# Performance work log

Hardware: AMD Instinct MI355X
Metric: run time of the kernel (lower is better)

## Reference

```python
import jax, jax.numpy as jnp
import numpy as np

T, D, N, K, H = 4096, 2560, 8, 4, 256
QUERY_PRE_ATTN_SCALAR = 256.0
ROPE_THETA = 10000.0
RMS_EPS = 1e-6
SLIDING_WINDOW = 1024
NEG_INF = -1e30


def setup_inputs() -> dict:
    key = jax.random.key(0)
    ks = jax.random.split(key, 6)
    return {
        "x": jax.random.normal(ks[0], (T, D), dtype=jnp.float32),
        "wq": jax.random.normal(ks[1], (D, N, H), dtype=jnp.float32) * 0.02,
        "wk": jax.random.normal(ks[2], (D, K, H), dtype=jnp.float32) * 0.02,
        "wv": jax.random.normal(ks[3], (D, K, H), dtype=jnp.float32) * 0.02,
        "wo": jax.random.normal(ks[4], (N, H, D), dtype=jnp.float32) * 0.02,
        "q_norm_w": jnp.ones((H,), dtype=jnp.float32),
        "k_norm_w": jnp.ones((H,), dtype=jnp.float32),
        "positions": jnp.arange(T, dtype=jnp.int32),
    }


def rms_norm(x, w, eps=RMS_EPS):
    rms = jnp.sqrt(jnp.mean(x * x, axis=-1, keepdims=True) + eps)
    return w * (x / rms)


def apply_rope(x, positions, head_dim, theta):
    # x: [T, heads, H]; rotate-half RoPE
    half = head_dim // 2
    inv_freq = theta ** (-(jnp.arange(half, dtype=jnp.float32) * 2.0 / head_dim))
    ang = positions.astype(jnp.float32)[:, None] * inv_freq  # [T, half]
    sin = jnp.sin(ang)[:, None, :]
    cos = jnp.cos(ang)[:, None, :]
    x1, x2 = jnp.split(x, 2, axis=-1)
    return jnp.concatenate([x1 * cos - x2 * sin, x2 * cos + x1 * sin], axis=-1)


def reference(x, wq, wk, wv, wo, q_norm_w, k_norm_w, positions):
    # QKV projections (per-head)
    q = jnp.einsum('td,dnh->tnh', x, wq)            # [T, N, H]
    q = rms_norm(q, q_norm_w)
    q = q * (QUERY_PRE_ATTN_SCALAR ** -0.5)
    q = apply_rope(q, positions, H, ROPE_THETA)

    k = jnp.einsum('td,dkh->tkh', x, wk)            # [T, K, H]
    k = rms_norm(k, k_norm_w)
    k = apply_rope(k, positions, H, ROPE_THETA)

    v = jnp.einsum('td,dkh->tkh', x, wv)            # [T, K, H]

    # GQA sliding-window causal attention
    G = N // K
    qh = q.reshape(T, K, G, H)
    scores = jnp.einsum('tkgh,skh->kgts', qh, k)    # [K, G, T, T]
    pq = positions[:, None]
    pk = positions[None, :]
    mask = (pk <= pq) & (pq - pk < SLIDING_WINDOW)  # [T, T]
    scores = jnp.where(mask, scores, NEG_INF)
    p = jax.nn.softmax(scores, axis=-1)
    attn = jnp.einsum('kgts,skh->tkgh', p, v).reshape(T, N, H)

    o = jnp.einsum('tnh,nhd->td', attn, wo)         # [T, D]
    new_kv_cache = jnp.stack([k, v])                # [2, T, K, H]
    return new_kv_cache, o
```

## Files before the change

### kernel.cpp

```cpp
#include <hip/hip_runtime.h>
#include <stdint.h>

#define T_TOK 4096
#define DM    2560
#define NQ    8
#define NKV   4
#define HD    256
#define WIN   1024

using bf16x8 = __attribute__((ext_vector_type(8))) short;
using f32x4  = __attribute__((ext_vector_type(4))) float;
typedef unsigned short u16;

__device__ __forceinline__ u16 f2bf(float x) {
  union { float f; uint32_t u; } v; v.f = x;
  uint32_t u = v.u;
  return (u16)((u + 0x7fffu + ((u >> 16) & 1u)) >> 16);
}
__device__ __forceinline__ float bf2f(u16 b) {
  union { uint32_t u; float f; } v; v.u = ((uint32_t)b) << 16;
  return v.f;
}

__device__ __forceinline__ void async_cp16(const void* g, void* lds) {
  __builtin_amdgcn_global_load_lds(
      (const __attribute__((address_space(1))) uint32_t*)(uintptr_t)g,
      (__attribute__((address_space(3))) uint32_t*)(uint32_t)(uintptr_t)lds,
      16, 0, 0);
}

__global__ __launch_bounds__(256) void convert_f32_bf16(
    const float* __restrict__ in, u16* __restrict__ out, int n)
{
  for (int i = (blockIdx.x * 256 + threadIdx.x) * 8; i < n; i += gridDim.x * 256 * 8) {
    float4 a = *(const float4*)(in + i);
    float4 b = *(const float4*)(in + i + 4);
    bf16x8 o;
    o[0] = (short)f2bf(a.x); o[1] = (short)f2bf(a.y);
    o[2] = (short)f2bf(a.z); o[3] = (short)f2bf(a.w);
    o[4] = (short)f2bf(b.x); o[5] = (short)f2bf(b.y);
    o[6] = (short)f2bf(b.z); o[7] = (short)f2bf(b.w);
    *(bf16x8*)(out + i) = o;
  }
}

__global__ __launch_bounds__(256) void transpose_f32_bf16(
    const float* __restrict__ in, u16* __restrict__ out, int R, int C)
{
  __shared__ u16 tile[64][72];
  const int r0 = blockIdx.y * 64, c0 = blockIdx.x * 64;
  const int tr = threadIdx.x >> 6, tc = threadIdx.x & 63;
  #pragma unroll
  for (int i = 0; i < 16; ++i) {
    int r = tr + i * 4;
    tile[r][tc] = f2bf(in[(size_t)(r0 + r) * C + c0 + tc]);
  }
  __syncthreads();
  const int oc = threadIdx.x >> 3, ch = threadIdx.x & 7;
  #pragma unroll
  for (int h = 0; h < 2; ++h) {
    const int c = oc + h * 32;
    bf16x8 v;
    #pragma unroll
    for (int j = 0; j < 8; ++j) v[j] = (short)tile[ch * 8 + j][c];
    *(bf16x8*)(out + (size_t)(c0 + c) * R + r0 + ch * 8) = v;
  }
}

template<bool F32OUT>
__global__ __launch_bounds__(512, 1) void gemm256p(
    const u16* __restrict__ A, const u16* __restrict__ B, void* __restrict__ Cv,
    int Kd, int lda, int ldb, int ldc)
{
  __shared__ __align__(16) u16 lds[2][2][256 * 64];
  const int tid = threadIdx.x;
  const int wave = tid >> 6, lane = tid & 63;
  const int lg = lane >> 4, lc = lane & 15;
  const int wr = wave >> 2, wc = wave & 3;
  const int nwg = gridDim.x, bid = blockIdx.x;
  const int nid = (bid & 7) * (nwg >> 3) + (bid >> 3);
  const int m0 = (nid & 15) * 256, n0 = (nid >> 4) * 256;
  const int NT = Kd >> 6;

  const int srow = tid >> 3;
  const int scol = ((tid & 7) * 16) ^ ((srow & 7) << 4);
  const u16* Ag = A + (size_t)(m0 + srow) * lda + (scol >> 1);
  const u16* Bg = B + (size_t)(n0 + srow) * ldb + (scol >> 1);

  #define STAGE_B4(BUF, KT) do {                                              \
    const int kc_ = (KT) * 64;                                                \
    _Pragma("unroll")                                                         \
    for (int li = 0; li < 4; ++li)                                            \
      async_cp16(Bg + (size_t)(li * 64) * ldb + kc_,                          \
                 (char*)&lds[BUF][1][0] + li * 8192 + wave * 1024);           \
  } while (0)
  #define STAGE_A2(BUF, KT, H) do {                                           \
    const int kc_ = (KT) * 64;                                                \
    async_cp16(Ag + (size_t)((H) * 64) * lda + kc_,                           \
               (char*)&lds[BUF][0][0] + (H) * 8192 + wave * 1024);            \
    async_cp16(Ag + (size_t)((H) * 64 + 128) * lda + kc_,                     \
               (char*)&lds[BUF][0][0] + ((H) + 2) * 8192 + wave * 1024);      \
  } while (0)
  #define LOAD_AF(P) do {                                                     \
    _Pragma("unroll")                                                         \
    for (int im = 0; im < 2; ++im)                                            \
      _Pragma("unroll")                                                       \
      for (int k2 = 0; k2 < 2; ++k2) {                                        \
        const int row = wr * 128 + ((P) * 2 + im) * 16 + lc;                  \
        const int cb = k2 * 64 + lg * 16;                                     \
        af[im][k2] = *(const bf16x8*)(Ab + row * 128 + (cb ^ ((row & 7) << 4))); \
      }                                                                       \
  } while (0)
  #define MFMA_Q(P) do {                                                      \
    __builtin_amdgcn_s_setprio(1);                                            \
    _Pragma("unroll")                                                         \
    for (int im = 0; im < 2; ++im)                                            \
      _Pragma("unroll")                                                       \
      for (int j = 0; j < 4; ++j)                                             \
        _Pragma("unroll")                                                     \
        for (int k2 = 0; k2 < 2; ++k2)                                        \
          acc[(P) * 2 + im][j] = __builtin_amdgcn_mfma_f32_16x16x32_bf16(     \
              af[im][k2], bfr[j][k2], acc[(P) * 2 + im][j], 0, 0, 0);         \
    __builtin_amdgcn_s_setprio(0);                                            \
  } while (0)
  #define LGKM0_BAR() do {                                                    \
    asm volatile("s_waitcnt lgkmcnt(0)" ::: "memory");                        \
    __builtin_amdgcn_s_barrier();                                             \
    __builtin_amdgcn_sched_barrier(0);                                        \
  } while (0)

  const f32x4 zf = {0.f, 0.f, 0.f, 0.f};
  f32x4 acc[8][4];
  #pragma unroll
  for (int i = 0; i < 8; ++i)
    #pragma unroll
    for (int j = 0; j < 4; ++j) acc[i][j] = zf;

  STAGE_B4(0, 0); STAGE_A2(0, 0, 0); STAGE_A2(0, 0, 1);
  STAGE_B4(1, 1); STAGE_A2(1, 1, 0); STAGE_A2(1, 1, 1);
  asm volatile("s_waitcnt vmcnt(8)" ::: "memory");
  __builtin_amdgcn_s_barrier();
  __builtin_amdgcn_sched_barrier(0);

  for (int t = 0; t < NT; ++t) {
    const int cur = t & 1;
    const char* Ab = (const char*)&lds[cur][0][0];
    const char* Bb = (const char*)&lds[cur][1][0];
    int nk = t + 2; if (nk > NT - 1) nk = NT - 1;

    bf16x8 bfr[4][2], af[2][2];
    #pragma unroll
    for (int j = 0; j < 4; ++j)
      #pragma unroll
      for (int k2 = 0; k2 < 2; ++k2) {
        const int row = wc * 64 + j * 16 + lc;
        const int cb = k2 * 64 + lg * 16;
        bfr[j][k2] = *(const bf16x8*)(Bb + row * 128 + (cb ^ ((row & 7) << 4)));
      }
    LOAD_AF(0);
    LGKM0_BAR();
    STAGE_B4(cur, nk);
    MFMA_Q(0);
    LOAD_AF(1);
    LGKM0_BAR();
    STAGE_A2(cur, nk, 0);
    MFMA_Q(1);
    LOAD_AF(2);
    MFMA_Q(2);
    LOAD_AF(3);
    LGKM0_BAR();
    STAGE_A2(cur, nk, 1);
    MFMA_Q(3);
    asm volatile("s_waitcnt vmcnt(8)" ::: "memory");
    __builtin_amdgcn_s_barrier();
    __builtin_amdgcn_sched_barrier(0);
  }
  #undef STAGE_B4
  #undef STAGE_A2
  #undef LOAD_AF
  #undef MFMA_Q
  #undef LGKM0_BAR

  #pragma unroll
  for (int i = 0; i < 8; ++i)
    #pragma unroll
    for (int j = 0; j < 4; ++j)
      #pragma unroll
      for (int r = 0; r < 4; ++r) {
        const int row = m0 + wr * 128 + i * 16 + lg * 4 + r;
        const int col = n0 + wc * 64 + j * 16 + lc;
        if (F32OUT) ((float*)Cv)[(size_t)row * ldc + col] = acc[i][j][r];
        else        ((u16*)Cv)[(size_t)row * ldc + col] = f2bf(acc[i][j][r]);
      }
}

__global__ __launch_bounds__(512, 1) void gemm_p2(
    const u16* __restrict__ A, const u16* __restrict__ B, float* __restrict__ C,
    int Kd, int lda, int ldb, int ldc)
{
  __shared__ __align__(16) u16 lds[2][(128 + 320) * 64];
  const int tid = threadIdx.x;
  const int wave = tid >> 6, lane = tid & 63;
  const int lg = lane >> 4, lc = lane & 15;
  const int wr = wave >> 2, wc = wave & 3;
  const int nwg = gridDim.x, bid = blockIdx.x;
  const int nid = (bid & 7) * (nwg >> 3) + (bid >> 3);
  const int m0 = (nid & 31) * 128, n0 = (nid >> 5) * 320;
  const int NT = Kd >> 6;

  const int srow = tid >> 3;
  const int scol = ((tid & 7) * 16) ^ ((srow & 7) << 4);
  const u16* Ag = A + (size_t)(m0 + srow) * lda + (scol >> 1);
  const u16* Bg = B + (size_t)(n0 + srow) * ldb + (scol >> 1);

  #define STAGE_B5(BUF, KT) do {                                              \
    const int kc_ = (KT) * 64;                                                \
    _Pragma("unroll")                                                         \
    for (int li = 0; li < 5; ++li)                                            \
      async_cp16(Bg + (size_t)(li * 64) * ldb + kc_,                          \
                 (char*)&lds[BUF][0] + 16384 + li * 8192 + wave * 1024);      \
  } while (0)
  #define STAGE_A2P(BUF, KT) do {                                             \
    const int kc_ = (KT) * 64;                                                \
    _Pragma("unroll")                                                         \
    for (int li = 0; li < 2; ++li)                                            \
      async_cp16(Ag + (size_t)(li * 64) * lda + kc_,                          \
                 (char*)&lds[BUF][0] + li * 8192 + wave * 1024);              \
  } while (0)
  #define LOAD_AF2(P) do {                                                    \
    _Pragma("unroll")                                                         \
    for (int im = 0; im < 2; ++im)                                            \
      _Pragma("unroll")                                                       \
      for (int k2 = 0; k2 < 2; ++k2) {                                        \
        const int row = wr * 64 + ((P) * 2 + im) * 16 + lc;                   \
        const int cb = k2 * 64 + lg * 16;                                     \
        af[im][k2] = *(const bf16x8*)(Ab + row * 128 + (cb ^ ((row & 7) << 4))); \
      }                                                                       \
  } while (0)
  #define MFMA_Q2(P) do {                                                     \
    __builtin_amdgcn_s_setprio(1);                                            \
    _Pragma("unroll")                                                         \
    for (int im = 0; im < 2; ++im)                                            \
      _Pragma("unroll")                                                       \
      for (int j = 0; j < 5; ++j)                                             \
        _Pragma("unroll")                                                     \
        for (int k2 = 0; k2 < 2; ++k2)                                        \
          acc[(P) * 2 + im][j] = __builtin_amdgcn_mfma_f32_16x16x32_bf16(     \
              af[im][k2], bfr[j][k2], acc[(P) * 2 + im][j], 0, 0, 0);         \
    __builtin_amdgcn_s_setprio(0);                                            \
  } while (0)
  #define LGKM0_BAR2() do {                                                   \
    asm volatile("s_waitcnt lgkmcnt(0)" ::: "memory");                        \
    __builtin_amdgcn_s_barrier();                                             \
    __builtin_amdgcn_sched_barrier(0);                                        \
  } while (0)

  const f32x4 zf = {0.f, 0.f, 0.f, 0.f};
  f32x4 acc[4][5];
  #pragma unroll
  for (int i = 0; i < 4; ++i)
    #pragma unroll
    for (int j = 0; j < 5; ++j) acc[i][j] = zf;

  STAGE_B5(0, 0); STAGE_A2P(0, 0);
  STAGE_B5(1, 1); STAGE_A2P(1, 1);
  asm volatile("s_waitcnt vmcnt(7)" ::: "memory");
  __builtin_amdgcn_s_barrier();
  __builtin_amdgcn_sched_barrier(0);

  for (int t = 0; t < NT; ++t) {
    const int cur = t & 1;
    const char* Ab = (const char*)&lds[cur][0];
    const char* Bb = Ab + 16384;
    int nk = t + 2; if (nk > NT - 1) nk = NT - 1;

    bf16x8 bfr[5][2], af[2][2];
    #pragma unroll
    for (int j = 0; j < 5; ++j)
      #pragma unroll
      for (int k2 = 0; k2 < 2; ++k2) {
        const int row = wc * 80 + j * 16 + lc;
        const int cb = k2 * 64 + lg * 16;
        bfr[j][k2] = *(const bf16x8*)(Bb + row * 128 + (cb ^ ((row & 7) << 4)));
      }
    LOAD_AF2(0);
    LGKM0_BAR2();
    STAGE_B5(cur, nk);
    MFMA_Q2(0);
    LOAD_AF2(1);
    LGKM0_BAR2();
    STAGE_A2P(cur, nk);
    MFMA_Q2(1);
    asm volatile("s_waitcnt vmcnt(7)" ::: "memory");
    __builtin_amdgcn_s_barrier();
    __builtin_amdgcn_sched_barrier(0);
  }
  #undef STAGE_B5
  #undef STAGE_A2P
  #undef LOAD_AF2
  #undef MFMA_Q2
  #undef LGKM0_BAR2

  #pragma unroll
  for (int i = 0; i < 4; ++i)
    #pragma unroll
    for (int j = 0; j < 5; ++j)
      #pragma unroll
      for (int r = 0; r < 4; ++r) {
        const int row = m0 + wr * 64 + i * 16 + lg * 4 + r;
        const int col = n0 + wc * 80 + j * 16 + lc;
        C[(size_t)row * ldc + col] = acc[i][j][r];
      }
}

__global__ __launch_bounds__(256) void fuse_norm_rope(
    const u16* __restrict__ qkv, const float* __restrict__ qnw, const float* __restrict__ knw,
    const int* __restrict__ pos, u16* __restrict__ qb, u16* __restrict__ kb,
    u16* __restrict__ vb, float* __restrict__ kvout)
{
  const int t = blockIdx.x;
  const int wave = threadIdx.x >> 6, lane = threadIdx.x & 63;
  const float p = (float)pos[t];
  const float kf = 0.10381025296523007f;
  float s0, c0, s1, c1;
  sincosf(p * exp2f(-(float)lane * kf), &s0, &c0);
  sincosf(p * exp2f(-(float)(lane + 64) * kf), &s1, &c1);
  const u16* row = qkv + (size_t)t * 4096;

  for (int pp = 0; pp < 4; ++pp) {
    const int hr = pp * 4 + wave;
    if (hr >= 12) {
      const int kk = hr - 12;
      const u16* src = row + 3072 + kk * 256;
      float* dstf = kvout + (size_t)T_TOK * NKV * HD + ((size_t)t * NKV + kk) * HD;
      u16*   dstb = vb + ((size_t)t * NKV + kk) * HD;
      #pragma unroll
      for (int q4 = 0; q4 < 4; ++q4) {
        const u16 s = src[lane + q4 * 64];
        dstf[lane + q4 * 64] = bf2f(s);
        dstb[lane + q4 * 64] = s;
      }
    } else {
      const bool isq = hr < 8;
      const int cb = isq ? hr * 256 : 2048 + (hr - 8) * 256;
      float v0 = bf2f(row[cb + lane]);
      float v1 = bf2f(row[cb + lane + 64]);
      float v2 = bf2f(row[cb + lane + 128]);
      float v3 = bf2f(row[cb + lane + 192]);
      float ss = v0 * v0 + v1 * v1 + v2 * v2 + v3 * v3;
      #pragma unroll
      for (int off = 1; off < 64; off <<= 1) ss += __shfl_xor(ss, off);
      float sc = rsqrtf(ss * (1.0f / 256.0f) + 1e-6f);
      if (isq) sc *= 0.0625f;
      const float* wn = isq ? qnw : knw;
      v0 *= sc * wn[lane];
      v1 *= sc * wn[lane + 64];
      v2 *= sc * wn[lane + 128];
      v3 *= sc * wn[lane + 192];
      const float n0 = v0 * c0 - v2 * s0;
      const float n2 = v2 * c0 + v0 * s0;
      const float n1 = v1 * c1 - v3 * s1;
      const float n3 = v3 * c1 + v1 * s1;
      if (isq) {
        u16* dst = qb + (size_t)t * 2048 + hr * 256;
        dst[lane]       = f2bf(n0);
        dst[lane + 64]  = f2bf(n1);
        dst[lane + 128] = f2bf(n2);
        dst[lane + 192] = f2bf(n3);
      } else {
        const int kk = hr - 8;
        float* dstf = kvout + ((size_t)t * NKV + kk) * HD;
        dstf[lane]       = n0;
        dstf[lane + 64]  = n1;
        dstf[lane + 128] = n2;
        dstf[lane + 192] = n3;
        u16* dstb = kb + ((size_t)t * NKV + kk) * HD;
        dstb[lane]       = f2bf(n0);
        dstb[lane + 64]  = f2bf(n1);
        dstb[lane + 128] = f2bf(n2);
        dstb[lane + 192] = f2bf(n3);
      }
    }
  }
}

__global__ __launch_bounds__(256) void transpose_v(
    const u16* __restrict__ vc, u16* __restrict__ vt)
{
  __shared__ u16 tile[64][72];
  const int kk = blockIdx.z;
  const int t0 = blockIdx.y * 64, h0 = blockIdx.x * 64;
  const int lr = threadIdx.x >> 3, ch = threadIdx.x & 7;
  #pragma unroll
  for (int h = 0; h < 2; ++h) {
    const int row = lr + h * 32;
    *(bf16x8*)&tile[row][ch * 8] =
        *(const bf16x8*)&vc[((size_t)(t0 + row) * NKV + kk) * HD + h0 + ch * 8];
  }
  __syncthreads();
  #pragma unroll
  for (int h = 0; h < 2; ++h) {
    const int hc = lr + h * 32;
    bf16x8 v;
    #pragma unroll
    for (int j = 0; j < 8; ++j) v[j] = (short)tile[ch * 8 + j][hc];
    *(bf16x8*)&vt[(size_t)kk * HD * T_TOK + (size_t)(h0 + hc) * T_TOK + t0 + ch * 8] = v;
  }
}

__global__ __launch_bounds__(512, 1) void attn_kernel(
    const u16* __restrict__ qb, const u16* __restrict__ kc,
    const u16* __restrict__ vt, u16* __restrict__ ob)
{
  __shared__ __align__(16) u16 Ks[2][64 * 256];
  __shared__ __align__(16) u16 Vts[2][256 * 64];
  __shared__ __align__(16) u16 Ps[8][16 * 64];

  const int kk = blockIdx.y;
  const int t0 = blockIdx.x * 64;
  const int tid = threadIdx.x;
  const int wave = tid >> 6, lane = tid & 63;
  const int lg = lane >> 4, lc = lane & 15;
  const int hq = kk * 2 + (wave >> 2);
  const int wrow = (wave & 3) * 16;
  const int lswz = (lc & 7) << 4;
  const f32x4 zf = {0.f, 0.f, 0.f, 0.f};

  const int lrowK = tid >> 5;
  const int scolK = ((tid & 31) * 16) ^ ((lrowK & 7) << 4);
  const int lrowV = tid >> 3;
  const int scolV = ((tid & 7) * 16) ^ ((lrowV & 7) << 4);

  #define STAGEKV(KT, BUF) do {                                                \
    const int kb_ = (KT) * 64;                                                 \
    const u16* kp_ = kc + (size_t)(kb_ + lrowK) * (NKV * HD) + kk * HD + (scolK >> 1); \
    _Pragma("unroll")                                                          \
    for (int is = 0; is < 4; ++is)                                             \
      async_cp16(kp_ + (size_t)(is * 16) * (NKV * HD),                         \
                 (char*)&Ks[BUF][0] + is * 8192 + wave * 1024);                \
    const u16* vp_ = vt + (size_t)kk * (HD * T_TOK) + (size_t)lrowV * T_TOK + kb_ + (scolV >> 1); \
    _Pragma("unroll")                                                          \
    for (int is = 0; is < 4; ++is)                                             \
      async_cp16(vp_ + (size_t)(is * 64) * T_TOK,                              \
                 (char*)&Vts[BUF][0] + is * 8192 + wave * 1024);               \
  } while (0)

  bf16x8 qf[8];
  {
    const u16* qp = qb + (size_t)(t0 + wrow + lc) * 2048 + hq * 256 + lg * 8;
    #pragma unroll
    for (int ks = 0; ks < 8; ++ks) qf[ks] = *(const bf16x8*)(qp + ks * 32);
  }

  f32x4 o_acc[16];
  #pragma unroll
  for (int j = 0; j < 16; ++j) o_acc[j] = zf;
  float m_r[4], l_r[4];
  #pragma unroll
  for (int r = 0; r < 4; ++r) { m_r[r] = -1e30f; l_r[r] = 0.f; }

  const int mtile = t0 >> 6;
  const int ktf = (mtile >= 16) ? (mtile - 16) : 0;

  STAGEKV(ktf, 0);
  __syncthreads();

  int cur = 0;
  for (int kt = ktf; kt <= mtile; ++kt) {
    const int kb = kt * 64;
    if (kt < mtile) STAGEKV(kt + 1, cur ^ 1);

    const u16* Kb = &Ks[cur][0];
    const u16* Vb = &Vts[cur][0];

    f32x4 sf[4];
    #pragma unroll
    for (int j = 0; j < 4; ++j) sf[j] = zf;
    __builtin_amdgcn_s_setprio(1);
    #pragma unroll
    for (int ks = 0; ks < 8; ++ks)
      #pragma unroll
      for (int j = 0; j < 4; ++j) {
        const int row = j * 16 + lc;
        bf16x8 kf = *(const bf16x8*)((const char*)Kb + ((row * 512 + ks * 64 + lg * 16) ^ lswz));
        sf[j] = __builtin_amdgcn_mfma_f32_16x16x32_bf16(qf[ks], kf, sf[j], 0, 0, 0);
      }
    __builtin_amdgcn_s_setprio(0);

    const bool interior = (kb >= t0 - 960) && (kb <= t0 - 64);
    if (!interior) {
      #pragma unroll
      for (int j = 0; j < 4; ++j) {
        const int gcol = kb + j * 16 + lc;
        #pragma unroll
        for (int r = 0; r < 4; ++r) {
          const int grow = t0 + wrow + lg * 4 + r;
          if ((unsigned)(grow - gcol) >= WIN) sf[j][r] = -1e30f;
        }
      }
    }

    float a_r[4];
    #pragma unroll
    for (int r = 0; r < 4; ++r) {
      float v = fmaxf(fmaxf(sf[0][r], sf[1][r]), fmaxf(sf[2][r], sf[3][r]));
      v = fmaxf(v, __shfl_xor(v, 1));
      v = fmaxf(v, __shfl_xor(v, 2));
      v = fmaxf(v, __shfl_xor(v, 4));
      v = fmaxf(v, __shfl_xor(v, 8));
      const float mn = fmaxf(m_r[r], v);
      a_r[r] = __expf(m_r[r] - mn);
      m_r[r] = mn;
    }

    char* myP = (char*)&Ps[wave][0];
    #pragma unroll
    for (int r = 0; r < 4; ++r) {
      const int row = lg * 4 + r;
      const int rsw = (row & 7) << 4;
      float su = 0.f;
      #pragma unroll
      for (int j = 0; j < 4; ++j) {
        const float p = __expf(sf[j][r] - m_r[r]);
        su += p;
        *(u16*)(myP + ((row * 128 + (j * 16 + lc) * 2) ^ rsw)) = f2bf(p);
      }
      su += __shfl_xor(su, 1);
      su += __shfl_xor(su, 2);
      su += __shfl_xor(su, 4);
      su += __shfl_xor(su, 8);
      l_r[r] = l_r[r] * a_r[r] + su;
    }

    #pragma unroll
    for (int j = 0; j < 16; ++j) {
      o_acc[j][0] *= a_r[0];
      o_acc[j][1] *= a_r[1];
      o_acc[j][2] *= a_r[2];
      o_acc[j][3] *= a_r[3];
    }

    bf16x8 pa[2];
    #pragma unroll
    for (int ks = 0; ks < 2; ++ks)
      pa[ks] = *(const bf16x8*)(myP + ((lc * 128 + ks * 64 + lg * 16) ^ lswz));
    __builtin_amdgcn_s_setprio(1);
    #pragma unroll
    for (int ks = 0; ks < 2; ++ks)
      #pragma unroll
      for (int j = 0; j < 16; ++j) {
        const int row = j * 16 + lc;
        bf16x8 vf = *(const bf16x8*)((const char*)Vb + ((row * 128 + ks * 64 + lg * 16) ^ lswz));
        o_acc[j] = __builtin_amdgcn_mfma_f32_16x16x32_bf16(pa[ks], vf, o_acc[j], 0, 0, 0);
      }
    __builtin_amdgcn_s_setprio(0);

    __syncthreads();
    cur ^= 1;
  }
  #undef STAGEKV

  #pragma unroll
  for (int r = 0; r < 4; ++r) {
    const float li = 1.f / l_r[r];
    const size_t rowb = (size_t)(t0 + wrow + lg * 4 + r) * 2048 + hq * 256 + lc;
    #pragma unroll
    for (int j = 0; j < 16; ++j)
      ob[rowb + j * 16] = f2bf(o_acc[j][r] * li);
  }
}

extern "C" void kernel_launch(void* const* d_in, const int* in_sizes, int n_in,
                              void* d_out, int out_size, void* d_ws, size_t ws_size,
                              hipStream_t stream)
{
  (void)in_sizes; (void)n_in; (void)out_size; (void)ws_size;
  const float* x   = (const float*)d_in[0];
  const float* wq  = (const float*)d_in[1];
  const float* wk  = (const float*)d_in[2];
  const float* wv  = (const float*)d_in[3];
  const float* wo  = (const float*)d_in[4];
  const float* qnw = (const float*)d_in[5];
  const float* knw = (const float*)d_in[6];
  const int*   pos = (const int*)d_in[7];
  float* out = (float*)d_out;

  char* ws = (char*)d_ws;
  u16* woT   = (u16*)(ws);
  u16* xb    = (u16*)(ws + 10485760);
  u16* wqkvT = (u16*)(ws + 31457280);
  u16* qkv   = (u16*)(ws + 52428800);
  u16* q_b   = xb;
  u16* kb    = wqkvT;
  u16* vb    = (u16*)(ws + 31457280 + 8388608);
  u16* vtb   = qkv;
  u16* attn  = (u16*)(ws + 52428800 + 8388608);

  convert_f32_bf16<<<1024, 256, 0, stream>>>(x, xb, T_TOK * DM);
  transpose_f32_bf16<<<dim3(32, 40), 256, 0, stream>>>(wq, wqkvT, DM, 2048);
  transpose_f32_bf16<<<dim3(16, 40), 256, 0, stream>>>(wk, wqkvT + 2048 * DM, DM, 1024);
  transpose_f32_bf16<<<dim3(16, 40), 256, 0, stream>>>(wv, wqkvT + 3072 * DM, DM, 1024);
  transpose_f32_bf16<<<dim3(40, 32), 256, 0, stream>>>(wo, woT, 2048, DM);

  gemm256p<false><<<256, 512, 0, stream>>>(xb, wqkvT, qkv, DM, DM, DM, 4096);

  fuse_norm_rope<<<T_TOK, 256, 0, stream>>>(qkv, qnw, knw, pos, q_b, kb, vb, out);

  transpose_v<<<dim3(4, 64, 4), 256, 0, stream>>>(vb, vtb);

  attn_kernel<<<dim3(64, 4), 512, 0, stream>>>(q_b, kb, vtb, attn);

  gemm_p2<<<256, 512, 0, stream>>>(attn, woT, out + 2 * (size_t)T_TOK * NKV * HD,
                                   2048, 2048, 2048, DM);
}
```

Measured before the change: 250.3 us.

## Load all A fragments upfront and issue whole-tile staging after one barrier

Both projection GEMM kernels stop interleaving LDS fragment loads, barriers and partial global staging across quarter or half MFMA groups. Each K-step now reads every A and B fragment into registers, does one lgkmcnt wait and barrier, issues all async copies for tile t+2 at once, and then runs the full MFMA block. This removes the extra intra-iteration barriers, at the cost of more VGPRs for the A fragments and less overlap between LDS reads and MFMA work.

Result: no change. 252.8 us (+1.0%).

```diff
diff --git a/kernel.cpp b/kernel.cpp
--- a/kernel.cpp
+++ b/kernel.cpp
@@ -87,46 +87,16 @@
   const u16* Ag = A + (size_t)(m0 + srow) * lda + (scol >> 1);
   const u16* Bg = B + (size_t)(n0 + srow) * ldb + (scol >> 1);
 
-  #define STAGE_B4(BUF, KT) do {                                              \
+  #define STAGE_ALL(BUF, KT) do {                                             \
     const int kc_ = (KT) * 64;                                                \
     _Pragma("unroll")                                                         \
     for (int li = 0; li < 4; ++li)                                            \
       async_cp16(Bg + (size_t)(li * 64) * ldb + kc_,                          \
                  (char*)&lds[BUF][1][0] + li * 8192 + wave * 1024);           \
-  } while (0)
-  #define STAGE_A2(BUF, KT, H) do {                                           \
-    const int kc_ = (KT) * 64;                                                \
-    async_cp16(Ag + (size_t)((H) * 64) * lda + kc_,                           \
-               (char*)&lds[BUF][0][0] + (H) * 8192 + wave * 1024);            \
-    async_cp16(Ag + (size_t)((H) * 64 + 128) * lda + kc_,                     \
-               (char*)&lds[BUF][0][0] + ((H) + 2) * 8192 + wave * 1024);      \
-  } while (0)
-  #define LOAD_AF(P) do {                                                     \
     _Pragma("unroll")                                                         \
-    for (int im = 0; im < 2; ++im)                                            \
-      _Pragma("unroll")                                                       \
-      for (int k2 = 0; k2 < 2; ++k2) {                                        \
-        const int row = wr * 128 + ((P) * 2 + im) * 16 + lc;                  \
-        const int cb = k2 * 64 + lg * 16;                                     \
-        af[im][k2] = *(const bf16x8*)(Ab + row * 128 + (cb ^ ((row & 7) << 4))); \
-      }                                                                       \
-  } while (0)
-  #define MFMA_Q(P) do {                                                      \
-    __builtin_amdgcn_s_setprio(1);                                            \
-    _Pragma("unroll")                                                         \
-    for (int im = 0; im < 2; ++im)                                            \
-      _Pragma("unroll")                                                       \
-      for (int j = 0; j < 4; ++j)                                             \
-        _Pragma("unroll")                                                     \
-        for (int k2 = 0; k2 < 2; ++k2)                                        \
-          acc[(P) * 2 + im][j] = __builtin_amdgcn_mfma_f32_16x16x32_bf16(     \
-              af[im][k2], bfr[j][k2], acc[(P) * 2 + im][j], 0, 0, 0);         \
-    __builtin_amdgcn_s_setprio(0);                                            \
-  } while (0)
-  #define LGKM0_BAR() do {                                                    \
-    asm volatile("s_waitcnt lgkmcnt(0)" ::: "memory");                        \
-    __builtin_amdgcn_s_barrier();                                             \
-    __builtin_amdgcn_sched_barrier(0);                                        \
+    for (int li = 0; li < 4; ++li)                                            \
+      async_cp16(Ag + (size_t)(li * 64) * lda + kc_,                          \
+                 (char*)&lds[BUF][0][0] + li * 8192 + wave * 1024);           \
   } while (0)
 
   const f32x4 zf = {0.f, 0.f, 0.f, 0.f};
@@ -136,8 +106,8 @@
     #pragma unroll
     for (int j = 0; j < 4; ++j) acc[i][j] = zf;
 
-  STAGE_B4(0, 0); STAGE_A2(0, 0, 0); STAGE_A2(0, 0, 1);
-  STAGE_B4(1, 1); STAGE_A2(1, 1, 0); STAGE_A2(1, 1, 1);
+  STAGE_ALL(0, 0);
+  STAGE_ALL(1, 1);
   asm volatile("s_waitcnt vmcnt(8)" ::: "memory");
   __builtin_amdgcn_s_barrier();
   __builtin_amdgcn_sched_barrier(0);
@@ -148,7 +118,7 @@
     const char* Bb = (const char*)&lds[cur][1][0];
     int nk = t + 2; if (nk > NT - 1) nk = NT - 1;
 
-    bf16x8 bfr[4][2], af[2][2];
+    bf16x8 bfr[4][2], af8[8][2];
     #pragma unroll
     for (int j = 0; j < 4; ++j)
       #pragma unroll
@@ -157,29 +127,33 @@
         const int cb = k2 * 64 + lg * 16;
         bfr[j][k2] = *(const bf16x8*)(Bb + row * 128 + (cb ^ ((row & 7) << 4)));
       }
-    LOAD_AF(0);
-    LGKM0_BAR();
-    STAGE_B4(cur, nk);
-    MFMA_Q(0);
-    LOAD_AF(1);
-    LGKM0_BAR();
-    STAGE_A2(cur, nk, 0);
-    MFMA_Q(1);
-    LOAD_AF(2);
-    MFMA_Q(2);
-    LOAD_AF(3);
-    LGKM0_BAR();
-    STAGE_A2(cur, nk, 1);
-    MFMA_Q(3);
+    #pragma unroll
+    for (int i = 0; i < 8; ++i)
+      #pragma unroll
+      for (int k2 = 0; k2 < 2; ++k2) {
+        const int row = wr * 128 + i * 16 + lc;
+        const int cb = k2 * 64 + lg * 16;
+        af8[i][k2] = *(const bf16x8*)(Ab + row * 128 + (cb ^ ((row & 7) << 4)));
+      }
+    asm volatile("s_waitcnt lgkmcnt(0)" ::: "memory");
+    __builtin_amdgcn_s_barrier();
+    __builtin_amdgcn_sched_barrier(0);
+    STAGE_ALL(cur, nk);
+    __builtin_amdgcn_s_setprio(1);
+    #pragma unroll
+    for (int i = 0; i < 8; ++i)
+      #pragma unroll
+      for (int j = 0; j < 4; ++j)
+        #pragma unroll
+        for (int k2 = 0; k2 < 2; ++k2)
+          acc[i][j] = __builtin_amdgcn_mfma_f32_16x16x32_bf16(
+              af8[i][k2], bfr[j][k2], acc[i][j], 0, 0, 0);
+    __builtin_amdgcn_s_setprio(0);
     asm volatile("s_waitcnt vmcnt(8)" ::: "memory");
     __builtin_amdgcn_s_barrier();
     __builtin_amdgcn_sched_barrier(0);
   }
-  #undef STAGE_B4
-  #undef STAGE_A2
-  #undef LOAD_AF
-  #undef MFMA_Q
-  #undef LGKM0_BAR
+  #undef STAGE_ALL
 
   #pragma unroll
   for (int i = 0; i < 8; ++i)
@@ -213,47 +187,17 @@
   const u16* Ag = A + (size_t)(m0 + srow) * lda + (scol >> 1);
   const u16* Bg = B + (size_t)(n0 + srow) * ldb + (scol >> 1);
 
-  #define STAGE_B5(BUF, KT) do {                                              \
+  #define STAGE_ALL2(BUF, KT) do {                                            \
     const int kc_ = (KT) * 64;                                                \
     _Pragma("unroll")                                                         \
     for (int li = 0; li < 5; ++li)                                            \
       async_cp16(Bg + (size_t)(li * 64) * ldb + kc_,                          \
                  (char*)&lds[BUF][0] + 16384 + li * 8192 + wave * 1024);      \
-  } while (0)
-  #define STAGE_A2P(BUF, KT) do {                                             \
-    const int kc_ = (KT) * 64;                                                \
     _Pragma("unroll")                                                         \
     for (int li = 0; li < 2; ++li)                                            \
       async_cp16(Ag + (size_t)(li * 64) * lda + kc_,                          \
                  (char*)&lds[BUF][0] + li * 8192 + wave * 1024);              \
   } while (0)
-  #define LOAD_AF2(P) do {                                                    \
-    _Pragma("unroll")                                                         \
-    for (int im = 0; im < 2; ++im)                                            \
-      _Pragma("unroll")                                                       \
-      for (int k2 = 0; k2 < 2; ++k2) {                                        \
-        const int row = wr * 64 + ((P) * 2 + im) * 16 + lc;                   \
-        const int cb = k2 * 64 + lg * 16;                                     \
-        af[im][k2] = *(const bf16x8*)(Ab + row * 128 + (cb ^ ((row & 7) << 4))); \
-      }                                                                       \
-  } while (0)
-  #define MFMA_Q2(P) do {                                                     \
-    __builtin_amdgcn_s_setprio(1);                                            \
-    _Pragma("unroll")                                                         \
-    for (int im = 0; im < 2; ++im)                                            \
-      _Pragma("unroll")                                                       \
-      for (int j = 0; j < 5; ++j)                                             \
-        _Pragma("unroll")                                                     \
-        for (int k2 = 0; k2 < 2; ++k2)                                        \
-          acc[(P) * 2 + im][j] = __builtin_amdgcn_mfma_f32_16x16x32_bf16(     \
-              af[im][k2], bfr[j][k2], acc[(P) * 2 + im][j], 0, 0, 0);         \
-    __builtin_amdgcn_s_setprio(0);                                            \
-  } while (0)
-  #define LGKM0_BAR2() do {                                                   \
-    asm volatile("s_waitcnt lgkmcnt(0)" ::: "memory");                        \
-    __builtin_amdgcn_s_barrier();                                             \
-    __builtin_amdgcn_sched_barrier(0);                                        \
-  } while (0)
 
   const f32x4 zf = {0.f, 0.f, 0.f, 0.f};
   f32x4 acc[4][5];
@@ -262,8 +206,8 @@
     #pragma unroll
     for (int j = 0; j < 5; ++j) acc[i][j] = zf;
 
-  STAGE_B5(0, 0); STAGE_A2P(0, 0);
-  STAGE_B5(1, 1); STAGE_A2P(1, 1);
+  STAGE_ALL2(0, 0);
+  STAGE_ALL2(1, 1);
   asm volatile("s_waitcnt vmcnt(7)" ::: "memory");
   __builtin_amdgcn_s_barrier();
   __builtin_amdgcn_sched_barrier(0);
@@ -274,7 +218,7 @@
     const char* Bb = Ab + 16384;
     int nk = t + 2; if (nk > NT - 1) nk = NT - 1;
 
-    bf16x8 bfr[5][2], af[2][2];
+    bf16x8 bfr[5][2], af4[4][2];
     #pragma unroll
     for (int j = 0; j < 5; ++j)
       #pragma unroll
@@ -283,23 +227,33 @@
         const int cb = k2 * 64 + lg * 16;
         bfr[j][k2] = *(const bf16x8*)(Bb + row * 128 + (cb ^ ((row & 7) << 4)));
       }
-    LOAD_AF2(0);
-    LGKM0_BAR2();
-    STAGE_B5(cur, nk);
-    MFMA_Q2(0);
-    LOAD_AF2(1);
-    LGKM0_BAR2();
-    STAGE_A2P(cur, nk);
-    MFMA_Q2(1);
+    #pragma unroll
+    for (int i = 0; i < 4; ++i)
+      #pragma unroll
+      for (int k2 = 0; k2 < 2; ++k2) {
+        const int row = wr * 64 + i * 16 + lc;
+        const int cb = k2 * 64 + lg * 16;
+        af4[i][k2] = *(const bf16x8*)(Ab + row * 128 + (cb ^ ((row & 7) << 4)));
+      }
+    asm volatile("s_waitcnt lgkmcnt(0)" ::: "memory");
+    __builtin_amdgcn_s_barrier();
+    __builtin_amdgcn_sched_barrier(0);
+    STAGE_ALL2(cur, nk);
+    __builtin_amdgcn_s_setprio(1);
+    #pragma unroll
+    for (int i = 0; i < 4; ++i)
+      #pragma unroll
+      for (int j = 0; j < 5; ++j)
+        #pragma unroll
+        for (int k2 = 0; k2 < 2; ++k2)
+          acc[i][j] = __builtin_amdgcn_mfma_f32_16x16x32_bf16(
+              af4[i][k2], bfr[j][k2], acc[i][j], 0, 0, 0);
+    __builtin_amdgcn_s_setprio(0);
     asm volatile("s_waitcnt vmcnt(7)" ::: "memory");
     __builtin_amdgcn_s_barrier();
     __builtin_amdgcn_sched_barrier(0);
   }
-  #undef STAGE_B5
-  #undef STAGE_A2P
-  #undef LOAD_AF2
-  #undef MFMA_Q2
-  #undef LGKM0_BAR2
+  #undef STAGE_ALL2
 
   #pragma unroll
   for (int i = 0; i < 4; ++i)
```

## Restructure 256x256 GEMM mainloop into eight-phase quadrant pipeline with finer-grained staging

Applied to the files above, without the earlier changes.

Reorganizes the 256x256 bf16 GEMM so each wave computes four 64x32 sub-tiles, one per 128x128 quadrant, instead of one 128x64 block. The K loop now advances two K tiles per iteration through eight phases. Each phase reads one quadrant's fragments from LDS, issues one half-tile of async global->LDS staging, then runs a short MFMA burst, which interleaves loads and compute more finely. This adds a barrier per phase and more LDS fragment reads per MFMA, since A and B fragments are reloaded for each quadrant, in exchange for smoother overlap of memory traffic and compute.

Measured after the change: 255.6 us. 2.1% more time.

```diff
diff --git a/kernel.cpp b/kernel.cpp
--- a/kernel.cpp
+++ b/kernel.cpp
@@ -87,111 +87,108 @@
   const u16* Ag = A + (size_t)(m0 + srow) * lda + (scol >> 1);
   const u16* Bg = B + (size_t)(n0 + srow) * ldb + (scol >> 1);
 
-  #define STAGE_B4(BUF, KT) do {                                              \
+  #define STG_A(H, BUF, KT) do {                                              \
     const int kc_ = (KT) * 64;                                                \
+    async_cp16(Ag + (size_t)((H) * 128) * lda + kc_,                          \
+               (char*)&lds[BUF][0][0] + (H) * 16384 + wave * 1024);           \
+    async_cp16(Ag + (size_t)((H) * 128 + 64) * lda + kc_,                     \
+               (char*)&lds[BUF][0][0] + (H) * 16384 + 8192 + wave * 1024);    \
+  } while (0)
+  #define STG_B(H, BUF, KT) do {                                              \
+    const int kc_ = (KT) * 64;                                                \
+    async_cp16(Bg + (size_t)((H) * 128) * ldb + kc_,                          \
+               (char*)&lds[BUF][1][0] + (H) * 16384 + wave * 1024);           \
+    async_cp16(Bg + (size_t)((H) * 128 + 64) * ldb + kc_,                     \
+               (char*)&lds[BUF][1][0] + (H) * 16384 + 8192 + wave * 1024);    \
+  } while (0)
+
+  const f32x4 zf = {0.f, 0.f, 0.f, 0.f};
+  f32x4 acc[2][2][4][2];
+  #pragma unroll
+  for (int qi = 0; qi < 2; ++qi)
+    #pragma unroll
+    for (int qj = 0; qj < 2; ++qj)
+      #pragma unroll
+      for (int mi = 0; mi < 4; ++mi)
+        #pragma unroll
+        for (int nj = 0; nj < 2; ++nj) acc[qi][qj][mi][nj] = zf;
+
+  #define PHASE(BUF, QI, QJ, STG) do {                                        \
+    const char* Ab_ = (const char*)&lds[BUF][0][0];                           \
+    const char* Bb_ = (const char*)&lds[BUF][1][0];                           \
+    bf16x8 af[4][2], bfm[2][2];                                               \
     _Pragma("unroll")                                                         \
-    for (int li = 0; li < 4; ++li)                                            \
-      async_cp16(Bg + (size_t)(li * 64) * ldb + kc_,                          \
-                 (char*)&lds[BUF][1][0] + li * 8192 + wave * 1024);           \
-  } while (0)
-  #define STAGE_A2(BUF, KT, H) do {                                           \
-    const int kc_ = (KT) * 64;                                                \
-    async_cp16(Ag + (size_t)((H) * 64) * lda + kc_,                           \
-               (char*)&lds[BUF][0][0] + (H) * 8192 + wave * 1024);            \
-    async_cp16(Ag + (size_t)((H) * 64 + 128) * lda + kc_,                     \
-               (char*)&lds[BUF][0][0] + ((H) + 2) * 8192 + wave * 1024);      \
-  } while (0)
-  #define LOAD_AF(P) do {                                                     \
-    _Pragma("unroll")                                                         \
-    for (int im = 0; im < 2; ++im)                                            \
+    for (int mi = 0; mi < 4; ++mi)                                            \
       _Pragma("unroll")                                                       \
       for (int k2 = 0; k2 < 2; ++k2) {                                        \
-        const int row = wr * 128 + ((P) * 2 + im) * 16 + lc;                  \
+        const int row = (QI) * 128 + wr * 64 + mi * 16 + lc;                  \
         const int cb = k2 * 64 + lg * 16;                                     \
-        af[im][k2] = *(const bf16x8*)(Ab + row * 128 + (cb ^ ((row & 7) << 4))); \
+        af[mi][k2] = *(const bf16x8*)(Ab_ + row * 128 + (cb ^ ((row & 7) << 4))); \
       }                                                                       \
-  } while (0)
-  #define MFMA_Q(P) do {                                                      \
+    _Pragma("unroll")                                                         \
+    for (int nj = 0; nj < 2; ++nj)                                            \
+      _Pragma("unroll")                                                       \
+      for (int k2 = 0; k2 < 2; ++k2) {                                        \
+        const int row = (QJ) * 128 + wc * 32 + nj * 16 + lc;                  \
+        const int cb = k2 * 64 + lg * 16;                                     \
+        bfm[nj][k2] = *(const bf16x8*)(Bb_ + row * 128 + (cb ^ ((row & 7) << 4))); \
+      }                                                                       \
+    STG;                                                                      \
+    asm volatile("s_waitcnt vmcnt(6)" ::: "memory");                          \
+    __builtin_amdgcn_s_barrier();                                             \
+    __builtin_amdgcn_sched_barrier(0);                                        \
     __builtin_amdgcn_s_setprio(1);                                            \
     _Pragma("unroll")                                                         \
-    for (int im = 0; im < 2; ++im)                                            \
+    for (int mi = 0; mi < 4; ++mi)                                            \
       _Pragma("unroll")                                                       \
-      for (int j = 0; j < 4; ++j)                                             \
+      for (int nj = 0; nj < 2; ++nj)                                          \
         _Pragma("unroll")                                                     \
         for (int k2 = 0; k2 < 2; ++k2)                                        \
-          acc[(P) * 2 + im][j] = __builtin_amdgcn_mfma_f32_16x16x32_bf16(     \
-              af[im][k2], bfr[j][k2], acc[(P) * 2 + im][j], 0, 0, 0);         \
+          acc[QI][QJ][mi][nj] = __builtin_amdgcn_mfma_f32_16x16x32_bf16(      \
+              af[mi][k2], bfm[nj][k2], acc[QI][QJ][mi][nj], 0, 0, 0);         \
     __builtin_amdgcn_s_setprio(0);                                            \
-  } while (0)
-  #define LGKM0_BAR() do {                                                    \
-    asm volatile("s_waitcnt lgkmcnt(0)" ::: "memory");                        \
     __builtin_amdgcn_s_barrier();                                             \
     __builtin_amdgcn_sched_barrier(0);                                        \
   } while (0)
 
-  const f32x4 zf = {0.f, 0.f, 0.f, 0.f};
-  f32x4 acc[8][4];
-  #pragma unroll
-  for (int i = 0; i < 8; ++i)
-    #pragma unroll
-    for (int j = 0; j < 4; ++j) acc[i][j] = zf;
-
-  STAGE_B4(0, 0); STAGE_A2(0, 0, 0); STAGE_A2(0, 0, 1);
-  STAGE_B4(1, 1); STAGE_A2(1, 1, 0); STAGE_A2(1, 1, 1);
-  asm volatile("s_waitcnt vmcnt(8)" ::: "memory");
+  STG_A(0, 0, 0); STG_A(1, 0, 0); STG_B(0, 0, 0); STG_B(1, 0, 0);
+  STG_A(0, 1, 1); STG_B(0, 1, 1);
+  asm volatile("s_waitcnt vmcnt(4)" ::: "memory");
   __builtin_amdgcn_s_barrier();
   __builtin_amdgcn_sched_barrier(0);
 
-  for (int t = 0; t < NT; ++t) {
-    const int cur = t & 1;
-    const char* Ab = (const char*)&lds[cur][0][0];
-    const char* Bb = (const char*)&lds[cur][1][0];
-    int nk = t + 2; if (nk > NT - 1) nk = NT - 1;
-
-    bf16x8 bfr[4][2], af[2][2];
-    #pragma unroll
-    for (int j = 0; j < 4; ++j)
-      #pragma unroll
-      for (int k2 = 0; k2 < 2; ++k2) {
-        const int row = wc * 64 + j * 16 + lc;
-        const int cb = k2 * 64 + lg * 16;
-        bfr[j][k2] = *(const bf16x8*)(Bb + row * 128 + (cb ^ ((row & 7) << 4)));
-      }
-    LOAD_AF(0);
-    LGKM0_BAR();
-    STAGE_B4(cur, nk);
-    MFMA_Q(0);
-    LOAD_AF(1);
-    LGKM0_BAR();
-    STAGE_A2(cur, nk, 0);
-    MFMA_Q(1);
-    LOAD_AF(2);
-    MFMA_Q(2);
-    LOAD_AF(3);
-    LGKM0_BAR();
-    STAGE_A2(cur, nk, 1);
-    MFMA_Q(3);
-    asm volatile("s_waitcnt vmcnt(8)" ::: "memory");
-    __builtin_amdgcn_s_barrier();
-    __builtin_amdgcn_sched_barrier(0);
-  }
-  #undef STAGE_B4
-  #undef STAGE_A2
-  #undef LOAD_AF
-  #undef MFMA_Q
-  #undef LGKM0_BAR
-
-  #pragma unroll
-  for (int i = 0; i < 8; ++i)
-    #pragma unroll
-    for (int j = 0; j < 4; ++j)
-      #pragma unroll
-      for (int r = 0; r < 4; ++r) {
-        const int row = m0 + wr * 128 + i * 16 + lg * 4 + r;
-        const int col = n0 + wc * 64 + j * 16 + lc;
-        if (F32OUT) ((float*)Cv)[(size_t)row * ldc + col] = acc[i][j][r];
-        else        ((u16*)Cv)[(size_t)row * ldc + col] = f2bf(acc[i][j][r]);
-      }
+  for (int it = 0; it < (NT >> 1); ++it) {
+    const int u = it * 2;
+    int u2 = u + 2; if (u2 > NT - 1) u2 = NT - 1;
+    int u3 = u + 3; if (u3 > NT - 1) u3 = NT - 1;
+    PHASE(0, 0, 0, STG_B(1, 1, u + 1));
+    PHASE(0, 0, 1, STG_A(1, 1, u + 1));
+    PHASE(0, 1, 0, STG_A(0, 0, u2));
+    PHASE(0, 1, 1, STG_B(0, 0, u2));
+    PHASE(1, 0, 0, STG_B(1, 0, u2));
+    PHASE(1, 0, 1, STG_A(1, 0, u2));
+    PHASE(1, 1, 0, STG_A(0, 1, u3));
+    PHASE(1, 1, 1, STG_B(0, 1, u3));
+  }
+  #undef PHASE
+  #undef STG_A
+  #undef STG_B
+
+  #pragma unroll
+  for (int qi = 0; qi < 2; ++qi)
+    #pragma unroll
+    for (int qj = 0; qj < 2; ++qj)
+      #pragma unroll
+      for (int mi = 0; mi < 4; ++mi)
+        #pragma unroll
+        for (int nj = 0; nj < 2; ++nj)
+          #pragma unroll
+          for (int r = 0; r < 4; ++r) {
+            const int row = m0 + qi * 128 + wr * 64 + mi * 16 + lg * 4 + r;
+            const int col = n0 + qj * 128 + wc * 32 + nj * 16 + lc;
+            if (F32OUT) ((float*)Cv)[(size_t)row * ldc + col] = acc[qi][qj][mi][nj][r];
+            else        ((u16*)Cv)[(size_t)row * ldc + col] = f2bf(acc[qi][qj][mi][nj][r]);
+          }
 }
 
 __global__ __launch_bounds__(512, 1) void gemm_p2(
```
